# Kernel tuning notes

Hardware: AMD Instinct MI355X
Metric: run time of the kernel (lower is better)

The kernel has to match this reference:

```python
import jax, jax.numpy as jnp
import numpy as np

B, T, H, D = 4, 2048, 16, 128
ATTN = H * D
FREQ_BASE = 10000.0


def _rope(t, base):
    # t: [B, T, H, D]; ggml-style interleaved RoPE on pairs (2i, 2i+1)
    d = t.shape[-1]
    seq = t.shape[1]
    pos = jnp.arange(seq, dtype=jnp.float32)                      # [T]
    inv_freq = base ** (-jnp.arange(0, d, 2, dtype=jnp.float32) / d)  # [D/2]
    ang = pos[:, None] * inv_freq[None, :]                        # [T, D/2]
    cos = jnp.cos(ang)[None, :, None, :]                          # [1,T,1,D/2]
    sin = jnp.sin(ang)[None, :, None, :]
    t1 = t[..., 0::2]
    t2 = t[..., 1::2]
    r1 = t1 * cos - t2 * sin
    r2 = t1 * sin + t2 * cos
    return jnp.stack([r1, r2], axis=-1).reshape(t.shape)


def setup_inputs() -> dict:
    key = jax.random.key(0)
    ks = jax.random.split(key, 12)
    s = 1.0 / np.sqrt(ATTN)
    return {
        "x": jax.random.normal(ks[0], (B, T, ATTN), dtype=jnp.float32),
        "freqs_cos": jax.random.normal(ks[1], (T, D // 2), dtype=jnp.float32),
        "freqs_sin": jax.random.normal(ks[2], (T, D // 2), dtype=jnp.float32),
        "wq_w": jax.random.normal(ks[3], (ATTN, ATTN), dtype=jnp.float32) * s,
        "wq_b": jax.random.normal(ks[4], (ATTN,), dtype=jnp.float32) * s,
        "wk_w": jax.random.normal(ks[5], (ATTN, ATTN), dtype=jnp.float32) * s,
        "wk_b": jax.random.normal(ks[6], (ATTN,), dtype=jnp.float32) * s,
        "wv_w": jax.random.normal(ks[7], (ATTN, ATTN), dtype=jnp.float32) * s,
        "wv_b": jax.random.normal(ks[8], (ATTN,), dtype=jnp.float32) * s,
        "wo_w": jax.random.normal(ks[9], (ATTN, ATTN), dtype=jnp.float32) * s,
        "wo_b": jax.random.normal(ks[10], (ATTN,), dtype=jnp.float32) * s,
    }


def reference(x, freqs_cos, freqs_sin, wq_w, wq_b, wk_w, wk_b, wv_w, wv_b, wo_w, wo_b):
    # freqs_cos / freqs_sin accepted for signature compatibility but ignored
    b, t, _ = x.shape
    q = (x @ wq_w.T + wq_b).reshape(b, t, H, D)
    k = (x @ wk_w.T + wk_b).reshape(b, t, H, D)
    v = (x @ wv_w.T + wv_b).reshape(b, t, H, D)
    q = _rope(q, FREQ_BASE)
    k = _rope(k, FREQ_BASE)
    # causal SDPA over [B, H, T, D]
    scale = 1.0 / np.sqrt(D).astype(np.float32)
    scores = jnp.einsum("bqhd,bkhd->bhqk", q, k) * scale          # [B,H,T,T]
    mask = jnp.tril(jnp.ones((t, t), dtype=bool))
    scores = jnp.where(mask[None, None], scores, jnp.finfo(scores.dtype).min)
    probs = jax.nn.softmax(scores, axis=-1)
    y = jnp.einsum("bhqk,bkhd->bqhd", probs, v).reshape(b, t, H * D)
    return y @ wo_w.T + wo_b
```

## Files before the change

### kernel.cpp

```cpp
#include <hip/hip_runtime.h>
#include <math.h>

#define Tt 2048
#define Hh 16
#define Dd 128
#define ATTN 2048

typedef unsigned short u16;
typedef __attribute__((ext_vector_type(8))) short short8;
typedef __attribute__((ext_vector_type(4))) float f32x4;

__device__ __forceinline__ float bf2f(u16 h) {
    union { unsigned int u; float f; } x;
    x.u = ((unsigned int)h) << 16;
    return x.f;
}
__device__ __forceinline__ u16 f2bf(float f) {
    union { float f; unsigned int u; } x;
    x.f = f;
    unsigned int r = x.u + 0x7fffu + ((x.u >> 16) & 1u);
    return (u16)(r >> 16);
}
__device__ __forceinline__ void gl_lds16(const void* g, void* l) {
    __builtin_amdgcn_global_load_lds(
        (const __attribute__((address_space(1))) unsigned int*)g,
        (__attribute__((address_space(3))) unsigned int*)l, 16, 0, 0);
}

__global__ __launch_bounds__(256) void freq_kernel(float* __restrict__ cost,
                                                   float* __restrict__ sint) {
    int idx = blockIdx.x * 256 + threadIdx.x;
    if (idx >= Tt * 64) return;
    int t = idx >> 6, i = idx & 63;
    double inv = exp(-((double)(2 * i) / 128.0) * log(10000.0));
    double ang = (double)t * inv;
    cost[idx] = (float)cos(ang);
    sint[idx] = (float)sin(ang);
}

__global__ __launch_bounds__(256) void cvt_kernel(const float* __restrict__ in,
                                                  u16* __restrict__ out, int n4) {
    int i = blockIdx.x * 256 + threadIdx.x;
    if (i >= n4) return;
    float4 v = *(const float4*)(in + (size_t)i * 4);
    union { ushort4 u; u16 s[4]; } pk;
    pk.s[0] = f2bf(v.x); pk.s[1] = f2bf(v.y);
    pk.s[2] = f2bf(v.z); pk.s[3] = f2bf(v.w);
    *(ushort4*)(out + (size_t)i * 4) = pk.u;
}

template<int MODE>
__global__ __launch_bounds__(256) void gemm_mfma(const u16* __restrict__ A,
                                                 const u16* __restrict__ W,
                                                 const float* __restrict__ bias,
                                                 void* __restrict__ Cout) {
    __shared__ u16 As[128 * 64];
    __shared__ u16 Ws[128 * 64];
    const int tid  = threadIdx.x;
    const int lane = tid & 63, w = tid >> 6;
    const int l15  = lane & 15, quad = lane >> 4;
    const int wm = w & 1, wn = w >> 1;

    const int id  = blockIdx.x + 16 * blockIdx.y;
    const int xcd = id & 7, j = id >> 3;
    const int by  = xcd * 8 + (j & 7);
    const int bx  = j >> 3;
    const int m0 = by * 128, n0 = bx * 128;

    const f32x4 zero4 = {0.f, 0.f, 0.f, 0.f};
    f32x4 acc[4][4];
#pragma unroll
    for (int mt = 0; mt < 4; mt++)
#pragma unroll
        for (int nt = 0; nt < 4; nt++) acc[mt][nt] = zero4;

    const int srow = w * 32 + (lane >> 3);
    const int gsc  = ((lane & 7) ^ (lane >> 3)) * 8;
    const u16* Ag = A + (size_t)(m0 + srow) * 2048 + gsc;
    const u16* Wg = W + (size_t)(n0 + srow) * 2048 + gsc;
    u16* AsW = As + w * 2048;
    u16* WsW = Ws + w * 2048;

    const int sw = l15 & 7;

    for (int k0 = 0; k0 < 2048; k0 += 64) {
        __syncthreads();
#pragma unroll
        for (int sub = 0; sub < 4; sub++)
            gl_lds16(Ag + (size_t)sub * 8 * 2048 + k0, AsW + sub * 512);
#pragma unroll
        for (int sub = 0; sub < 4; sub++)
            gl_lds16(Wg + (size_t)sub * 8 * 2048 + k0, WsW + sub * 512);
        __syncthreads();

        short8 af[4][2], bfr[4][2];
#pragma unroll
        for (int mt = 0; mt < 4; mt++)
#pragma unroll
            for (int kx = 0; kx < 2; kx++)
                af[mt][kx] = *(const short8*)(As + (wm * 64 + mt * 16 + l15) * 64 +
                                              (((kx * 4 + quad) ^ sw) * 8));
#pragma unroll
        for (int nt = 0; nt < 4; nt++)
#pragma unroll
            for (int kx = 0; kx < 2; kx++)
                bfr[nt][kx] = *(const short8*)(Ws + (wn * 64 + nt * 16 + l15) * 64 +
                                               (((kx * 4 + quad) ^ sw) * 8));
#pragma unroll
        for (int kx = 0; kx < 2; kx++)
#pragma unroll
            for (int mt = 0; mt < 4; mt++)
#pragma unroll
                for (int nt = 0; nt < 4; nt++)
                    acc[mt][nt] = __builtin_amdgcn_mfma_f32_16x16x32_bf16(
                        af[mt][kx], bfr[nt][kx], acc[mt][nt], 0, 0, 0);
    }

    float bn[4];
#pragma unroll
    for (int nt = 0; nt < 4; nt++) bn[nt] = bias[n0 + wn * 64 + nt * 16 + l15];

    if (MODE == 0) {
        float* C = (float*)Cout;
#pragma unroll
        for (int mt = 0; mt < 4; mt++) {
            int m = m0 + wm * 64 + mt * 16 + quad * 4;
#pragma unroll
            for (int nt = 0; nt < 4; nt++) {
                int n = n0 + wn * 64 + nt * 16 + l15;
#pragma unroll
                for (int r = 0; r < 4; r++)
                    C[(size_t)(m + r) * 2048 + n] = acc[mt][nt][r] + bn[nt];
            }
        }
    } else if (MODE == 1) {
        u16* C = (u16*)Cout;
        const int h = n0 >> 7;
#pragma unroll
        for (int mt = 0; mt < 4; mt++) {
            int m = m0 + wm * 64 + mt * 16 + quad * 4;
            int b = m >> 11, t = m & 2047;
            size_t base = ((size_t)(b * Hh + h) * Tt + t) * Dd;
#pragma unroll
            for (int nt = 0; nt < 4; nt++) {
                int d = wn * 64 + nt * 16 + l15;
#pragma unroll
                for (int r = 0; r < 4; r++)
                    C[base + (size_t)r * Dd + d] = f2bf(acc[mt][nt][r] + bn[nt]);
            }
        }
    } else {
        u16* C = (u16*)Cout;
        const int h = n0 >> 7;
        const int b = m0 >> 11;
        const int tb = (m0 & 2047) + wm * 64;
#pragma unroll
        for (int mt = 0; mt < 4; mt++) {
            int t4 = tb + mt * 16 + quad * 4;
#pragma unroll
            for (int nt = 0; nt < 4; nt++) {
                int d = wn * 64 + nt * 16 + l15;
                union { ushort4 u; u16 s[4]; } pk;
#pragma unroll
                for (int r = 0; r < 4; r++) pk.s[r] = f2bf(acc[mt][nt][r] + bn[nt]);
                *(ushort4*)&C[((size_t)(b * Hh + h) * Dd + d) * Tt + t4] = pk.u;
            }
        }
    }
}

#define QSCALE 0.12751743f
__global__ __launch_bounds__(256) void rope_kernel(u16* __restrict__ q,
                                                   u16* __restrict__ k,
                                                   const float* __restrict__ cost,
                                                   const float* __restrict__ sint) {
    int p = blockIdx.x * 256 + threadIdx.x;
    int g4 = (p & 15) * 4;
    int t  = (p >> 4) & 2047;
    float4 c4 = *(const float4*)(cost + t * 64 + g4);
    float4 s4 = *(const float4*)(sint + t * 64 + g4);
    float cc[4] = {c4.x, c4.y, c4.z, c4.w};
    float ss[4] = {s4.x, s4.y, s4.z, s4.w};
    size_t off = (size_t)p * 8;
    short8 qv = *(short8*)(q + off);
    short8 kv = *(short8*)(k + off);
    short8 qo, ko;
#pragma unroll
    for (int j = 0; j < 4; j++) {
        float q0 = bf2f((u16)qv[2 * j]), q1 = bf2f((u16)qv[2 * j + 1]);
        qo[2 * j]     = (short)f2bf((q0 * cc[j] - q1 * ss[j]) * QSCALE);
        qo[2 * j + 1] = (short)f2bf((q0 * ss[j] + q1 * cc[j]) * QSCALE);
        float k0 = bf2f((u16)kv[2 * j]), k1 = bf2f((u16)kv[2 * j + 1]);
        ko[2 * j]     = (short)f2bf(k0 * cc[j] - k1 * ss[j]);
        ko[2 * j + 1] = (short)f2bf(k0 * ss[j] + k1 * cc[j]);
    }
    *(short8*)(q + off) = qo;
    *(short8*)(k + off) = ko;
}

__global__ __launch_bounds__(256) void flash_mfma(const u16* __restrict__ Q,
                                                  const u16* __restrict__ K,
                                                  const u16* __restrict__ Vt,
                                                  u16* __restrict__ O) {
    __shared__ u16 Ks[64 * 128];
    __shared__ u16 Vs[128 * 64];
    __shared__ u16 Ps[4][32 * 72];
    __shared__ float als[4][32];
    __shared__ float lls[4][32];
    const int tid  = threadIdx.x;
    const int lane = tid & 63, w = tid >> 6;
    const int l15  = lane & 15, quad = lane >> 4;

    const int id  = blockIdx.x;
    const int bh  = (id & 7) * 8 + ((id >> 3) & 7);
    const int bxp = id >> 6;

    const u16* Kg[4]; const u16* Vg[4];
    u16* KsD[4]; u16* VsD[4];
#pragma unroll
    for (int cc = 0; cc < 4; cc++) {
        int kp = w * 16 + cc * 4 + quad;
        int gs = l15 ^ (cc * 4 + quad);
        Kg[cc]  = K + ((size_t)bh * Tt + kp) * Dd + gs * 8;
        KsD[cc] = Ks + (w * 4 + cc) * 512;
        int d  = w * 32 + cc * 8 + (lane >> 3);
        int gv = (lane & 7) ^ (lane >> 3);
        Vg[cc]  = Vt + ((size_t)bh * Dd + d) * Tt + gv * 8;
        VsD[cc] = Vs + (w * 4 + cc) * 512;
    }

    const f32x4 zero4 = {0.f, 0.f, 0.f, 0.f};

    for (int ph = 0; ph < 2; ph++) {
        const int qt = ph ? bxp : 15 - bxp;
        const int q0 = qt * 128;

        short8 qf[2][4];
        const u16* Qb = Q + ((size_t)bh * Tt + q0 + w * 32 + l15) * Dd + quad * 8;
#pragma unroll
        for (int nt = 0; nt < 2; nt++)
#pragma unroll
            for (int ks = 0; ks < 4; ks++)
                qf[nt][ks] = *(const short8*)(Qb + nt * 16 * Dd + ks * 32);

        f32x4 Oa[2][8];
#pragma unroll
        for (int mo = 0; mo < 2; mo++)
#pragma unroll
            for (int nt2 = 0; nt2 < 8; nt2++) Oa[mo][nt2] = zero4;
        float mrow[2] = {-INFINITY, -INFINITY};
        float lrow[2] = {0.f, 0.f};

        const int nkt = 2 * qt + 2;
        for (int kt = 0; kt < nkt; kt++) {
            __syncthreads();
#pragma unroll
            for (int cc = 0; cc < 4; cc++) gl_lds16(Kg[cc] + (size_t)kt * 64 * Dd, KsD[cc]);
#pragma unroll
            for (int cc = 0; cc < 4; cc++) gl_lds16(Vg[cc] + kt * 64, VsD[cc]);
            __syncthreads();

            if (kt * 64 > q0 + w * 32 + 31) continue;

            f32x4 sc[4][2];
#pragma unroll
            for (int mt = 0; mt < 4; mt++) { sc[mt][0] = zero4; sc[mt][1] = zero4; }
            __builtin_amdgcn_s_setprio(1);
#pragma unroll
            for (int ks = 0; ks < 4; ks++) {
                short8 kf[4];
#pragma unroll
                for (int mt = 0; mt < 4; mt++)
                    kf[mt] = *(const short8*)(Ks + (mt * 16 + l15) * 128 +
                                              (((ks * 4 + quad) ^ l15) * 8));
#pragma unroll
                for (int mt = 0; mt < 4; mt++) {
                    sc[mt][0] = __builtin_amdgcn_mfma_f32_16x16x32_bf16(kf[mt], qf[0][ks], sc[mt][0], 0, 0, 0);
                    sc[mt][1] = __builtin_amdgcn_mfma_f32_16x16x32_bf16(kf[mt], qf[1][ks], sc[mt][1], 0, 0, 0);
                }
            }
            __builtin_amdgcn_s_setprio(0);

            const bool diag = (kt * 64 + 63 > q0 + w * 32);
#pragma unroll
            for (int nt = 0; nt < 2; nt++) {
                const int q_g = q0 + w * 32 + nt * 16 + l15;
                float sv[16];
#pragma unroll
                for (int mt = 0; mt < 4; mt++)
#pragma unroll
                    for (int r = 0; r < 4; r++)
                        sv[mt * 4 + r] = sc[mt][nt][r];
                if (diag) {
#pragma unroll
                    for (int mt = 0; mt < 4; mt++)
#pragma unroll
                        for (int r = 0; r < 4; r++) {
                            int kp_g = kt * 64 + mt * 16 + quad * 4 + r;
                            if (kp_g > q_g) sv[mt * 4 + r] = -INFINITY;
                        }
                }
                float m8[8], m4[4];
#pragma unroll
                for (int e = 0; e < 8; e++) m8[e] = fmaxf(sv[e], sv[e + 8]);
#pragma unroll
                for (int e = 0; e < 4; e++) m4[e] = fmaxf(m8[e], m8[e + 4]);
                float mx = fmaxf(fmaxf(m4[0], m4[1]), fmaxf(m4[2], m4[3]));
                mx = fmaxf(mx, __shfl_xor(mx, 16, 64));
                mx = fmaxf(mx, __shfl_xor(mx, 32, 64));
                float mnew = fmaxf(mrow[nt], mx);
                mnew = (mnew - mrow[nt] <= 8.f) ? mrow[nt] : mnew;
                float alpha = exp2f(mrow[nt] - mnew);
                float pv[16];
#pragma unroll
                for (int e = 0; e < 16; e++) pv[e] = exp2f(sv[e] - mnew);
                float s8[8], s4[4];
#pragma unroll
                for (int e = 0; e < 8; e++) s8[e] = pv[e] + pv[e + 8];
#pragma unroll
                for (int e = 0; e < 4; e++) s4[e] = s8[e] + s8[e + 4];
                float rs = (s4[0] + s4[1]) + (s4[2] + s4[3]);
                rs += __shfl_xor(rs, 16, 64);
                rs += __shfl_xor(rs, 32, 64);
                lrow[nt] = lrow[nt] * alpha + rs;
                mrow[nt] = mnew;
                if (quad == 0) als[w][nt * 16 + l15] = alpha;
#pragma unroll
                for (int mt = 0; mt < 4; mt++) {
                    union { ushort4 u; u16 s[4]; } pk;
#pragma unroll
                    for (int r = 0; r < 4; r++) pk.s[r] = f2bf(pv[mt * 4 + r]);
                    *(ushort4*)&Ps[w][(nt * 16 + l15) * 72 + mt * 16 + quad * 4] = pk.u;
                }
            }

            float ao[2][4];
            bool need = false;
#pragma unroll
            for (int mo = 0; mo < 2; mo++)
#pragma unroll
                for (int r = 0; r < 4; r++) {
                    ao[mo][r] = als[w][mo * 16 + quad * 4 + r];
                    need |= (ao[mo][r] != 1.f);
                }
            if (__any(need)) {
#pragma unroll
                for (int mo = 0; mo < 2; mo++)
#pragma unroll
                    for (int nt2 = 0; nt2 < 8; nt2++)
#pragma unroll
                        for (int r = 0; r < 4; r++) Oa[mo][nt2][r] *= ao[mo][r];
            }

            __builtin_amdgcn_s_setprio(1);
#pragma unroll
            for (int ks2 = 0; ks2 < 2; ks2++) {
                short8 pf[2];
#pragma unroll
                for (int mo = 0; mo < 2; mo++)
                    pf[mo] = *(const short8*)&Ps[w][(mo * 16 + l15) * 72 + ks2 * 32 + quad * 8];
#pragma unroll
                for (int nt2 = 0; nt2 < 8; nt2++) {
                    short8 vf = *(const short8*)(Vs + (nt2 * 16 + l15) * 64 +
                                                 (((ks2 * 4 + quad) ^ (l15 & 7)) * 8));
                    Oa[0][nt2] = __builtin_amdgcn_mfma_f32_16x16x32_bf16(pf[0], vf, Oa[0][nt2], 0, 0, 0);
                    Oa[1][nt2] = __builtin_amdgcn_mfma_f32_16x16x32_bf16(pf[1], vf, Oa[1][nt2], 0, 0, 0);
                }
            }
            __builtin_amdgcn_s_setprio(0);
        }

        if (quad == 0) { lls[w][l15] = lrow[0]; lls[w][16 + l15] = lrow[1]; }
        float li[2][4];
#pragma unroll
        for (int mo = 0; mo < 2; mo++)
#pragma unroll
            for (int r = 0; r < 4; r++) li[mo][r] = 1.f / lls[w][mo * 16 + quad * 4 + r];
        const int b = bh >> 4, h = bh & 15;
#pragma unroll
        for (int mo = 0; mo < 2; mo++)
#pragma unroll
            for (int r = 0; r < 4; r++) {
                size_t ro = ((size_t)b * Tt + q0 + w * 32 + mo * 16 + quad * 4 + r) * ATTN
                            + h * Dd;
#pragma unroll
                for (int nt2 = 0; nt2 < 8; nt2++)
                    O[ro + nt2 * 16 + l15] = f2bf(Oa[mo][nt2][r] * li[mo][r]);
            }
    }
}

extern "C" void kernel_launch(void* const* d_in, const int* in_sizes, int n_in,
                              void* d_out, int out_size, void* d_ws, size_t ws_size,
                              hipStream_t stream) {
    const float* x    = (const float*)d_in[0];
    const float* wq_w = (const float*)d_in[3];
    const float* wq_b = (const float*)d_in[4];
    const float* wk_w = (const float*)d_in[5];
    const float* wk_b = (const float*)d_in[6];
    const float* wv_w = (const float*)d_in[7];
    const float* wv_b = (const float*)d_in[8];
    const float* wo_w = (const float*)d_in[9];
    const float* wo_b = (const float*)d_in[10];

    char* ws = (char*)d_ws;
    u16*   qb  = (u16*)(ws);
    u16*   kb  = (u16*)(ws + 33554432);
    u16*   vtb = (u16*)(ws + 67108864);
    u16*   xb  = (u16*)(ws + 100663296);
    u16*   obb = xb;
    u16*   wqb = (u16*)(ws + 134217728);
    u16*   wkb = (u16*)(ws + 142606336);
    u16*   wvb = (u16*)(ws + 150994944);
    u16*   wob = (u16*)(ws + 159383552);
    float* ct  = (float*)(ws + 167772160);
    float* st  = (float*)(ws + 168296448);

    freq_kernel<<<512, 256, 0, stream>>>(ct, st);
    cvt_kernel<<<16384, 256, 0, stream>>>(x, xb, 4194304);
    cvt_kernel<<<4096, 256, 0, stream>>>(wq_w, wqb, 1048576);
    cvt_kernel<<<4096, 256, 0, stream>>>(wk_w, wkb, 1048576);
    cvt_kernel<<<4096, 256, 0, stream>>>(wv_w, wvb, 1048576);
    cvt_kernel<<<4096, 256, 0, stream>>>(wo_w, wob, 1048576);

    dim3 gg(16, 64);
    gemm_mfma<1><<<gg, 256, 0, stream>>>(xb, wqb, wq_b, qb);
    gemm_mfma<1><<<gg, 256, 0, stream>>>(xb, wkb, wk_b, kb);
    gemm_mfma<2><<<gg, 256, 0, stream>>>(xb, wvb, wv_b, vtb);
    rope_kernel<<<8192, 256, 0, stream>>>(qb, kb, ct, st);
    flash_mfma<<<512, 256, 0, stream>>>(qb, kb, vtb, obb);
    gemm_mfma<0><<<gg, 256, 0, stream>>>(obb, wob, wo_b, (float*)d_out);
}
```

Measured before the change: 690.7 us.

## Restructure projection GEMMs into 256x256 tiles with double-buffered async LDS pipeline

The projection GEMMs move from 128x128 tiles with 256 threads to 256x256 tiles with 512 threads (8 waves), using 128KB of dynamic LDS split into two buffers. Global-to-LDS loads for the next k-step are issued while MFMAs run on the current buffer, with explicit vmcnt/lgkmcnt waits, split barriers and s_setprio around the MFMA blocks. The point is more data reuse per tile and hiding load latency that the old load-sync-compute loop exposed. In exchange, the grid becomes exactly 256 blocks (one per CU, one wave), occupancy drops to one block per CU, and the code depends on large dynamic LDS and hand-tuned wait counts.

```diff
diff --git a/kernel.cpp b/kernel.cpp
--- a/kernel.cpp
+++ b/kernel.cpp
@@ -50,71 +50,107 @@
 }
 
 template<int MODE>
-__global__ __launch_bounds__(256) void gemm_mfma(const u16* __restrict__ A,
-                                                 const u16* __restrict__ W,
-                                                 const float* __restrict__ bias,
-                                                 void* __restrict__ Cout) {
-    __shared__ u16 As[128 * 64];
-    __shared__ u16 Ws[128 * 64];
+__global__ __launch_bounds__(512, 2) void gemm_mfma(const u16* __restrict__ A,
+                                                    const u16* __restrict__ W,
+                                                    const float* __restrict__ bias,
+                                                    void* __restrict__ Cout) {
+    extern __shared__ u16 lds[];
     const int tid  = threadIdx.x;
     const int lane = tid & 63, w = tid >> 6;
     const int l15  = lane & 15, quad = lane >> 4;
-    const int wm = w & 1, wn = w >> 1;
-
-    const int id  = blockIdx.x + 16 * blockIdx.y;
-    const int xcd = id & 7, j = id >> 3;
-    const int by  = xcd * 8 + (j & 7);
-    const int bx  = j >> 3;
-    const int m0 = by * 128, n0 = bx * 128;
+    const int wm = w >> 2, wn = w & 3;
+
+    const int id = blockIdx.x;
+    const int bx = id & 7, by = id >> 3;
+    const int m0 = by * 256, n0 = bx * 256;
 
     const f32x4 zero4 = {0.f, 0.f, 0.f, 0.f};
-    f32x4 acc[4][4];
-#pragma unroll
-    for (int mt = 0; mt < 4; mt++)
+    f32x4 acc[8][4];
+#pragma unroll
+    for (int mt = 0; mt < 8; mt++)
 #pragma unroll
         for (int nt = 0; nt < 4; nt++) acc[mt][nt] = zero4;
 
-    const int srow = w * 32 + (lane >> 3);
+    const int srow = w * 16 + (lane >> 3);
     const int gsc  = ((lane & 7) ^ (lane >> 3)) * 8;
     const u16* Ag = A + (size_t)(m0 + srow) * 2048 + gsc;
     const u16* Wg = W + (size_t)(n0 + srow) * 2048 + gsc;
-    u16* AsW = As + w * 2048;
-    u16* WsW = Ws + w * 2048;
-
-    const int sw = l15 & 7;
-
-    for (int k0 = 0; k0 < 2048; k0 += 64) {
-        __syncthreads();
-#pragma unroll
-        for (int sub = 0; sub < 4; sub++)
-            gl_lds16(Ag + (size_t)sub * 8 * 2048 + k0, AsW + sub * 512);
-#pragma unroll
-        for (int sub = 0; sub < 4; sub++)
-            gl_lds16(Wg + (size_t)sub * 8 * 2048 + k0, WsW + sub * 512);
-        __syncthreads();
-
-        short8 af[4][2], bfr[4][2];
+    const int wB = w * 1024;
+
+    const int s7 = l15 & 7;
+    const int cA = wm * 8192 + l15 * 64;
+    const int cB = 16384 + (wn >> 1) * 8192 + ((wn & 1) * 64 + l15) * 64;
+    const int ck0 = (quad ^ s7) * 8;
+    const int ck1 = ((quad ^ s7) ^ 4) * 8;
+
+#define STAGE(tt, dd, ss) do { \
+    const u16* _g = (((ss) < 2) ? Ag : Wg) + (((ss) & 1) ? (size_t)(128 * 2048) : (size_t)0) \
+                    + (size_t)(tt) * 64; \
+    u16* _l = lds + (dd) * 32768 + (ss) * 8192 + wB; \
+    gl_lds16(_g, _l); \
+    gl_lds16(_g + (size_t)8 * 2048, _l + 512); \
+} while (0)
+
+    STAGE(0, 0, 0); STAGE(0, 0, 1); STAGE(0, 0, 2); STAGE(0, 0, 3);
+    STAGE(1, 1, 0); STAGE(1, 1, 1);
+
+    short8 af[4][2], bf[4][2];
+    for (int t = 0; t < 32; t++) {
+        const int d = t & 1, e = d ^ 1;
+        const u16* bufd = lds + d * 32768;
+
+        if (t < 31) { asm volatile("s_waitcnt vmcnt(4)" ::: "memory"); }
+        else        { asm volatile("s_waitcnt vmcnt(0)" ::: "memory"); }
+        __builtin_amdgcn_sched_barrier(0);
+        __builtin_amdgcn_s_barrier();
+        __builtin_amdgcn_sched_barrier(0);
+
+#pragma unroll
+        for (int mt = 0; mt < 4; mt++) {
+            af[mt][0] = *(const short8*)(bufd + cA + mt * 1024 + ck0);
+            af[mt][1] = *(const short8*)(bufd + cA + mt * 1024 + ck1);
+        }
+#pragma unroll
+        for (int nt = 0; nt < 4; nt++) {
+            bf[nt][0] = *(const short8*)(bufd + cB + nt * 1024 + ck0);
+            bf[nt][1] = *(const short8*)(bufd + cB + nt * 1024 + ck1);
+        }
+        if (t + 1 < 32) STAGE(t + 1, e, 2);
+        if (t + 1 < 32) STAGE(t + 1, e, 3);
+        __builtin_amdgcn_s_setprio(1);
 #pragma unroll
         for (int mt = 0; mt < 4; mt++)
 #pragma unroll
-            for (int kx = 0; kx < 2; kx++)
-                af[mt][kx] = *(const short8*)(As + (wm * 64 + mt * 16 + l15) * 64 +
-                                              (((kx * 4 + quad) ^ sw) * 8));
-#pragma unroll
-        for (int nt = 0; nt < 4; nt++)
-#pragma unroll
-            for (int kx = 0; kx < 2; kx++)
-                bfr[nt][kx] = *(const short8*)(Ws + (wn * 64 + nt * 16 + l15) * 64 +
-                                               (((kx * 4 + quad) ^ sw) * 8));
-#pragma unroll
-        for (int kx = 0; kx < 2; kx++)
-#pragma unroll
-            for (int mt = 0; mt < 4; mt++)
-#pragma unroll
-                for (int nt = 0; nt < 4; nt++)
-                    acc[mt][nt] = __builtin_amdgcn_mfma_f32_16x16x32_bf16(
-                        af[mt][kx], bfr[nt][kx], acc[mt][nt], 0, 0, 0);
+            for (int nt = 0; nt < 4; nt++) {
+                acc[mt][nt] = __builtin_amdgcn_mfma_f32_16x16x32_bf16(
+                    af[mt][0], bf[nt][0], acc[mt][nt], 0, 0, 0);
+                acc[mt][nt] = __builtin_amdgcn_mfma_f32_16x16x32_bf16(
+                    af[mt][1], bf[nt][1], acc[mt][nt], 0, 0, 0);
+            }
+        __builtin_amdgcn_s_setprio(0);
+#pragma unroll
+        for (int mt = 0; mt < 4; mt++) {
+            af[mt][0] = *(const short8*)(bufd + cA + (mt + 4) * 1024 + ck0);
+            af[mt][1] = *(const short8*)(bufd + cA + (mt + 4) * 1024 + ck1);
+        }
+        asm volatile("s_waitcnt lgkmcnt(0)" ::: "memory");
+        __builtin_amdgcn_sched_barrier(0);
+        __builtin_amdgcn_s_barrier();
+        __builtin_amdgcn_sched_barrier(0);
+        if (t + 2 < 32) { STAGE(t + 2, d, 0); STAGE(t + 2, d, 1); }
+        __builtin_amdgcn_s_setprio(1);
+#pragma unroll
+        for (int mt = 0; mt < 4; mt++)
+#pragma unroll
+            for (int nt = 0; nt < 4; nt++) {
+                acc[mt + 4][nt] = __builtin_amdgcn_mfma_f32_16x16x32_bf16(
+                    af[mt][0], bf[nt][0], acc[mt + 4][nt], 0, 0, 0);
+                acc[mt + 4][nt] = __builtin_amdgcn_mfma_f32_16x16x32_bf16(
+                    af[mt][1], bf[nt][1], acc[mt + 4][nt], 0, 0, 0);
+            }
+        __builtin_amdgcn_s_setprio(0);
     }
+#undef STAGE
 
     float bn[4];
 #pragma unroll
@@ -123,8 +159,8 @@
     if (MODE == 0) {
         float* C = (float*)Cout;
 #pragma unroll
-        for (int mt = 0; mt < 4; mt++) {
-            int m = m0 + wm * 64 + mt * 16 + quad * 4;
+        for (int mt = 0; mt < 8; mt++) {
+            int m = m0 + wm * 128 + mt * 16 + quad * 4;
 #pragma unroll
             for (int nt = 0; nt < 4; nt++) {
                 int n = n0 + wn * 64 + nt * 16 + l15;
@@ -135,35 +171,34 @@
         }
     } else if (MODE == 1) {
         u16* C = (u16*)Cout;
-        const int h = n0 >> 7;
-#pragma unroll
-        for (int mt = 0; mt < 4; mt++) {
-            int m = m0 + wm * 64 + mt * 16 + quad * 4;
-            int b = m >> 11, t = m & 2047;
-            size_t base = ((size_t)(b * Hh + h) * Tt + t) * Dd;
+#pragma unroll
+        for (int mt = 0; mt < 8; mt++) {
+            int m = m0 + wm * 128 + mt * 16 + quad * 4;
+            int b = m >> 11, tr = m & 2047;
 #pragma unroll
             for (int nt = 0; nt < 4; nt++) {
-                int d = wn * 64 + nt * 16 + l15;
+                int n = n0 + wn * 64 + nt * 16 + l15;
+                int h = n >> 7, dd = n & 127;
+                size_t base = ((size_t)(b * Hh + h) * Tt + tr) * Dd + dd;
 #pragma unroll
                 for (int r = 0; r < 4; r++)
-                    C[base + (size_t)r * Dd + d] = f2bf(acc[mt][nt][r] + bn[nt]);
+                    C[base + (size_t)r * Dd] = f2bf(acc[mt][nt][r] + bn[nt]);
             }
         }
     } else {
         u16* C = (u16*)Cout;
-        const int h = n0 >> 7;
         const int b = m0 >> 11;
-        const int tb = (m0 & 2047) + wm * 64;
-#pragma unroll
-        for (int mt = 0; mt < 4; mt++) {
-            int t4 = tb + mt * 16 + quad * 4;
+#pragma unroll
+        for (int mt = 0; mt < 8; mt++) {
+            int tloc = (m0 & 2047) + wm * 128 + mt * 16 + quad * 4;
 #pragma unroll
             for (int nt = 0; nt < 4; nt++) {
-                int d = wn * 64 + nt * 16 + l15;
+                int n = n0 + wn * 64 + nt * 16 + l15;
+                int h = n >> 7, dd = n & 127;
                 union { ushort4 u; u16 s[4]; } pk;
 #pragma unroll
                 for (int r = 0; r < 4; r++) pk.s[r] = f2bf(acc[mt][nt][r] + bn[nt]);
-                *(ushort4*)&C[((size_t)(b * Hh + h) * Dd + d) * Tt + t4] = pk.u;
+                *(ushort4*)&C[((size_t)(b * Hh + h) * Dd + dd) * Tt + tloc] = pk.u;
             }
         }
     }
@@ -423,11 +458,10 @@
     cvt_kernel<<<4096, 256, 0, stream>>>(wv_w, wvb, 1048576);
     cvt_kernel<<<4096, 256, 0, stream>>>(wo_w, wob, 1048576);
 
-    dim3 gg(16, 64);
-    gemm_mfma<1><<<gg, 256, 0, stream>>>(xb, wqb, wq_b, qb);
-    gemm_mfma<1><<<gg, 256, 0, stream>>>(xb, wkb, wk_b, kb);
-    gemm_mfma<2><<<gg, 256, 0, stream>>>(xb, wvb, wv_b, vtb);
+    gemm_mfma<1><<<256, 512, 131072, stream>>>(xb, wqb, wq_b, qb);
+    gemm_mfma<1><<<256, 512, 131072, stream>>>(xb, wkb, wk_b, kb);
+    gemm_mfma<2><<<256, 512, 131072, stream>>>(xb, wvb, wv_b, vtb);
     rope_kernel<<<8192, 256, 0, stream>>>(qb, kb, ct, st);
     flash_mfma<<<512, 256, 0, stream>>>(qb, kb, vtb, obb);
-    gemm_mfma<0><<<gg, 256, 0, stream>>>(obb, wob, wo_b, (float*)d_out);
-}
+    gemm_mfma<0><<<256, 512, 131072, stream>>>(obb, wob, wo_b, (float*)d_out);
+}
```

New measurement: 662.0 us. -4.2%, faster.
